# Kernel optimization log

Hardware: AMD Instinct MI355X
Metric: run time of the kernel (lower is better)

## Reference

```python
import jax, jax.numpy as jnp
import numpy as np


def setup_inputs() -> dict:
    key = jax.random.key(0)
    k1, k2, k3 = jax.random.split(key, 3)
    shape = (32, 3, 512, 512)
    inp = jax.random.normal(k1, shape, dtype=jnp.float32)
    tgt = jax.random.normal(k2, shape, dtype=jnp.float32)
    mask = jax.random.randint(k3, shape, 0, 2, dtype=jnp.int32)
    return {"input": inp, "target": tgt, "mask": mask}


def reference(input, target, mask):
    # masked MSE: mean of squared diff over elements where mask == 1
    diff2 = (input - target) ** 2
    m = (mask == 1).astype(diff2.dtype)
    sum2 = jnp.sum(diff2 * m)
    num = jnp.sum(m)
    return sum2 / num
```

## Files before the change

kernel.cpp:

```cpp
#include <hip/hip_runtime.h>


#define BLOCK 256
#define UNROLL 8
#define MAX_PARTS 8192

typedef float vfloat4 __attribute__((ext_vector_type(4)));
typedef int   vint4   __attribute__((ext_vector_type(4)));

__global__ __launch_bounds__(BLOCK, 2) void masked_mse_stage1(
    const vfloat4* __restrict__ inp,
    const vfloat4* __restrict__ tgt,
    const vint4* __restrict__ msk,
    float* __restrict__ part_sum,
    unsigned int* __restrict__ part_cnt)
{
    const long base = (long)blockIdx.x * (BLOCK * UNROLL) + threadIdx.x;

    vfloat4 a[UNROLL];
    vfloat4 b[UNROLL];
    vint4 m[UNROLL];
#pragma unroll
    for (int u = 0; u < UNROLL; ++u) {
        const long i = base + (long)u * BLOCK;
        a[u] = __builtin_nontemporal_load(&inp[i]);
        b[u] = __builtin_nontemporal_load(&tgt[i]);
        m[u] = __builtin_nontemporal_load(&msk[i]);
    }

    float s = 0.0f;
    unsigned int c = 0u;
#pragma unroll
    for (int u = 0; u < UNROLL; ++u) {
        float d0 = a[u].x - b[u].x;
        float d1 = a[u].y - b[u].y;
        float d2 = a[u].z - b[u].z;
        float d3 = a[u].w - b[u].w;
        s += (float)m[u].x * d0 * d0;
        s += (float)m[u].y * d1 * d1;
        s += (float)m[u].z * d2 * d2;
        s += (float)m[u].w * d3 * d3;
        c += (unsigned int)(m[u].x + m[u].y + m[u].z + m[u].w);
    }

#pragma unroll
    for (int off = 32; off > 0; off >>= 1) {
        s += __shfl_down(s, off, 64);
        c += __shfl_down(c, off, 64);
    }

    __shared__ float ssum[BLOCK / 64];
    __shared__ unsigned int scnt[BLOCK / 64];
    const int lane = threadIdx.x & 63;
    const int wave = threadIdx.x >> 6;
    if (lane == 0) {
        ssum[wave] = s;
        scnt[wave] = c;
    }
    __syncthreads();
    if (threadIdx.x == 0) {
        float bs = 0.0f;
        unsigned int bc = 0u;
#pragma unroll
        for (int w = 0; w < BLOCK / 64; ++w) {
            bs += ssum[w];
            bc += scnt[w];
        }
        part_sum[blockIdx.x] = bs;
        part_cnt[blockIdx.x] = bc;
    }
}

__global__ void masked_mse_tail(
    const float* __restrict__ inp,
    const float* __restrict__ tgt,
    const int* __restrict__ msk,
    float* __restrict__ part_sum,
    unsigned int* __restrict__ part_cnt,
    long start, long n, int tail_base)
{
    long i = start + blockIdx.x * (long)blockDim.x + threadIdx.x;
    float s = 0.0f;
    unsigned int c = 0u;
    for (; i < n; i += (long)gridDim.x * blockDim.x) {
        float d = inp[i] - tgt[i];
        int mv = msk[i];
        s += (float)mv * d * d;
        c += (unsigned int)mv;
    }
#pragma unroll
    for (int off = 32; off > 0; off >>= 1) {
        s += __shfl_down(s, off, 64);
        c += __shfl_down(c, off, 64);
    }
    __shared__ float ssum[4];
    __shared__ unsigned int scnt[4];
    const int lane = threadIdx.x & 63;
    const int wave = threadIdx.x >> 6;
    if (lane == 0) { ssum[wave] = s; scnt[wave] = c; }
    __syncthreads();
    if (threadIdx.x == 0) {
        float bs = 0.0f;
        unsigned int bc = 0u;
        for (int w = 0; w < (int)(blockDim.x / 64); ++w) { bs += ssum[w]; bc += scnt[w]; }
        part_sum[tail_base + blockIdx.x] = bs;
        part_cnt[tail_base + blockIdx.x] = bc;
    }
}

__global__ __launch_bounds__(1024) void masked_mse_stage2(
    const float* __restrict__ part_sum,
    const unsigned int* __restrict__ part_cnt,
    int nparts,
    float* __restrict__ out)
{
    float s = 0.0f;
    unsigned int c = 0u;
    for (int i = threadIdx.x; i < nparts; i += blockDim.x) {
        s += part_sum[i];
        c += part_cnt[i];
    }
#pragma unroll
    for (int off = 32; off > 0; off >>= 1) {
        s += __shfl_down(s, off, 64);
        c += __shfl_down(c, off, 64);
    }
    __shared__ float ssum[16];
    __shared__ unsigned int scnt[16];
    const int lane = threadIdx.x & 63;
    const int wave = threadIdx.x >> 6;
    if (lane == 0) { ssum[wave] = s; scnt[wave] = c; }
    __syncthreads();
    if (threadIdx.x == 0) {
        float ts = 0.0f;
        unsigned int tc = 0u;
#pragma unroll
        for (int w = 0; w < 16; ++w) { ts += ssum[w]; tc += scnt[w]; }
        out[0] = ts / (float)tc;
    }
}

extern "C" void kernel_launch(void* const* d_in, const int* in_sizes, int n_in,
                              void* d_out, int out_size, void* d_ws, size_t ws_size,
                              hipStream_t stream)
{
    const float* inp = (const float*)d_in[0];
    const float* tgt = (const float*)d_in[1];
    const int* msk = (const int*)d_in[2];
    const long n = in_sizes[0];
    const long n4 = n / 4;

    float* part_sum = (float*)d_ws;
    unsigned int* part_cnt = (unsigned int*)((char*)d_ws + MAX_PARTS * sizeof(float));

    const long per_block = (long)BLOCK * UNROLL;
    long nblocks = n4 / per_block;
    if (nblocks > MAX_PARTS - 64) nblocks = MAX_PARTS - 64;

    int nparts = 0;
    if (nblocks > 0) {
        masked_mse_stage1<<<(int)nblocks, BLOCK, 0, stream>>>(
            (const vfloat4*)inp, (const vfloat4*)tgt, (const vint4*)msk,
            part_sum, part_cnt);
        nparts = (int)nblocks;
    }
    const long covered = nblocks * per_block * 4;
    if (covered < n) {
        masked_mse_tail<<<64, BLOCK, 0, stream>>>(
            inp, tgt, msk, part_sum, part_cnt, covered, n, nparts);
        nparts += 64;
    }
    masked_mse_stage2<<<1, 1024, 0, stream>>>(part_sum, part_cnt, nparts, (float*)d_out);
}
```

Baseline: 246.6 us.

## Fuse final reduction into main kernel via hierarchical atomic tickets

Replaces the separate stage-2 reduction launch with a last-block-done pattern. Each block writes its partial sum and count as a packed float2 with an agent-scope atomic store, then takes a ticket from one of eight group counters and a second-level counter. The last block reads all partials and writes the mean. This removes a kernel launch and its gap, at the cost of a memset launch, per-block atomics and a serial final reduction in one block. Counts are now accumulated in float.

```diff
diff --git a/kernel.cpp b/kernel.cpp
--- a/kernel.cpp
+++ b/kernel.cpp
@@ -6,15 +6,39 @@
 #define MAX_PARTS 8192
 
 typedef float vfloat4 __attribute__((ext_vector_type(4)));
+typedef float vfloat2 __attribute__((ext_vector_type(2)));
 typedef int   vint4   __attribute__((ext_vector_type(4)));
 
-__global__ __launch_bounds__(BLOCK, 2) void masked_mse_stage1(
+__device__ __forceinline__ void store_part_agent(vfloat2* p, float s, float c)
+{
+    vfloat2 v; v.x = s; v.y = c;
+    unsigned long long u = __builtin_bit_cast(unsigned long long, v);
+    __hip_atomic_store((unsigned long long*)p, u, __ATOMIC_RELAXED,
+                       __HIP_MEMORY_SCOPE_AGENT);
+}
+__device__ __forceinline__ vfloat2 load_part_agent(const vfloat2* p)
+{
+    unsigned long long u = __hip_atomic_load((const unsigned long long*)p,
+                                             __ATOMIC_RELAXED,
+                                             __HIP_MEMORY_SCOPE_AGENT);
+    return __builtin_bit_cast(vfloat2, u);
+}
+
+template <int FINISH>
+__global__ __launch_bounds__(BLOCK, 2) void masked_mse_fused(
     const vfloat4* __restrict__ inp,
     const vfloat4* __restrict__ tgt,
     const vint4* __restrict__ msk,
-    float* __restrict__ part_sum,
-    unsigned int* __restrict__ part_cnt)
-{
+    vfloat2* __restrict__ parts,
+    unsigned int* __restrict__ tickets,
+    float* __restrict__ out)
+{
+    __shared__ float ssum[BLOCK / 64];
+    __shared__ unsigned int scnt[BLOCK / 64];
+    __shared__ int amLast;
+    __shared__ float f1[BLOCK / 64];
+    __shared__ float f2[BLOCK / 64];
+
     const long base = (long)blockIdx.x * (BLOCK * UNROLL) + threadIdx.x;
 
     vfloat4 a[UNROLL];
@@ -49,8 +73,6 @@
         c += __shfl_down(c, off, 64);
     }
 
-    __shared__ float ssum[BLOCK / 64];
-    __shared__ unsigned int scnt[BLOCK / 64];
     const int lane = threadIdx.x & 63;
     const int wave = threadIdx.x >> 6;
     if (lane == 0) {
@@ -58,6 +80,7 @@
         scnt[wave] = c;
     }
     __syncthreads();
+
     if (threadIdx.x == 0) {
         float bs = 0.0f;
         unsigned int bc = 0u;
@@ -66,8 +89,51 @@
             bs += ssum[w];
             bc += scnt[w];
         }
-        part_sum[blockIdx.x] = bs;
-        part_cnt[blockIdx.x] = bc;
+        store_part_agent(&parts[blockIdx.x], bs, (float)bc);
+
+        if (FINISH) {
+            const unsigned int g = blockIdx.x & 7u;
+            const unsigned int nb = gridDim.x;
+            const unsigned int gsz = nb / 8u + (g < (nb & 7u) ? 1u : 0u);
+            int last = 0;
+            unsigned int old = __hip_atomic_fetch_add(
+                &tickets[g], 1u, __ATOMIC_ACQ_REL, __HIP_MEMORY_SCOPE_AGENT);
+            if (old == gsz - 1u) {
+                const unsigned int ng = nb < 8u ? nb : 8u;
+                unsigned int o2 = __hip_atomic_fetch_add(
+                    &tickets[8], 1u, __ATOMIC_ACQ_REL, __HIP_MEMORY_SCOPE_AGENT);
+                last = (o2 == ng - 1u) ? 1 : 0;
+            }
+            amLast = last;
+        } else {
+            amLast = 0;
+        }
+    }
+
+    if (FINISH) {
+        __syncthreads();
+        if (amLast) {
+            float fs = 0.0f;
+            float fc = 0.0f;
+            for (unsigned int i = threadIdx.x; i < gridDim.x; i += BLOCK) {
+                vfloat2 p = load_part_agent(&parts[i]);
+                fs += p.x;
+                fc += p.y;
+            }
+#pragma unroll
+            for (int off = 32; off > 0; off >>= 1) {
+                fs += __shfl_down(fs, off, 64);
+                fc += __shfl_down(fc, off, 64);
+            }
+            if (lane == 0) { f1[wave] = fs; f2[wave] = fc; }
+            __syncthreads();
+            if (threadIdx.x == 0) {
+                float ts = 0.0f, tc = 0.0f;
+#pragma unroll
+                for (int w = 0; w < BLOCK / 64; ++w) { ts += f1[w]; tc += f2[w]; }
+                out[0] = ts / tc;
+            }
+        }
     }
 }
 
@@ -75,8 +141,7 @@
     const float* __restrict__ inp,
     const float* __restrict__ tgt,
     const int* __restrict__ msk,
-    float* __restrict__ part_sum,
-    unsigned int* __restrict__ part_cnt,
+    vfloat2* __restrict__ parts,
     long start, long n, int tail_base)
 {
     long i = start + blockIdx.x * (long)blockDim.x + threadIdx.x;
@@ -103,40 +168,39 @@
         float bs = 0.0f;
         unsigned int bc = 0u;
         for (int w = 0; w < (int)(blockDim.x / 64); ++w) { bs += ssum[w]; bc += scnt[w]; }
-        part_sum[tail_base + blockIdx.x] = bs;
-        part_cnt[tail_base + blockIdx.x] = bc;
-    }
-}
-
-__global__ __launch_bounds__(1024) void masked_mse_stage2(
-    const float* __restrict__ part_sum,
-    const unsigned int* __restrict__ part_cnt,
+        vfloat2 p; p.x = bs; p.y = (float)bc;
+        parts[tail_base + blockIdx.x] = p;
+    }
+}
+
+__global__ __launch_bounds__(256) void masked_mse_stage2(
+    const vfloat2* __restrict__ parts,
     int nparts,
     float* __restrict__ out)
 {
     float s = 0.0f;
-    unsigned int c = 0u;
+    float c = 0.0f;
     for (int i = threadIdx.x; i < nparts; i += blockDim.x) {
-        s += part_sum[i];
-        c += part_cnt[i];
+        vfloat2 p = parts[i];
+        s += p.x;
+        c += p.y;
     }
 #pragma unroll
     for (int off = 32; off > 0; off >>= 1) {
         s += __shfl_down(s, off, 64);
         c += __shfl_down(c, off, 64);
     }
-    __shared__ float ssum[16];
-    __shared__ unsigned int scnt[16];
+    __shared__ float ssum[4];
+    __shared__ float scnt[4];
     const int lane = threadIdx.x & 63;
     const int wave = threadIdx.x >> 6;
     if (lane == 0) { ssum[wave] = s; scnt[wave] = c; }
     __syncthreads();
     if (threadIdx.x == 0) {
-        float ts = 0.0f;
-        unsigned int tc = 0u;
-#pragma unroll
-        for (int w = 0; w < 16; ++w) { ts += ssum[w]; tc += scnt[w]; }
-        out[0] = ts / (float)tc;
+        float ts = 0.0f, tc = 0.0f;
+#pragma unroll
+        for (int w = 0; w < 4; ++w) { ts += ssum[w]; tc += scnt[w]; }
+        out[0] = ts / tc;
     }
 }
 
@@ -150,25 +214,34 @@
     const long n = in_sizes[0];
     const long n4 = n / 4;
 
-    float* part_sum = (float*)d_ws;
-    unsigned int* part_cnt = (unsigned int*)((char*)d_ws + MAX_PARTS * sizeof(float));
+    vfloat2* parts = (vfloat2*)d_ws;
+    unsigned int* tickets =
+        (unsigned int*)((char*)d_ws + (size_t)MAX_PARTS * sizeof(vfloat2));
 
     const long per_block = (long)BLOCK * UNROLL;
     long nblocks = n4 / per_block;
     if (nblocks > MAX_PARTS - 64) nblocks = MAX_PARTS - 64;
+    const long covered = nblocks * per_block * 4;
+
+    if (nblocks > 0 && covered == n) {
+        hipMemsetAsync(tickets, 0, 64, stream);
+        masked_mse_fused<1><<<(int)nblocks, BLOCK, 0, stream>>>(
+            (const vfloat4*)inp, (const vfloat4*)tgt, (const vint4*)msk,
+            parts, tickets, (float*)d_out);
+        return;
+    }
 
     int nparts = 0;
     if (nblocks > 0) {
-        masked_mse_stage1<<<(int)nblocks, BLOCK, 0, stream>>>(
+        masked_mse_fused<0><<<(int)nblocks, BLOCK, 0, stream>>>(
             (const vfloat4*)inp, (const vfloat4*)tgt, (const vint4*)msk,
-            part_sum, part_cnt);
+            parts, tickets, (float*)d_out);
         nparts = (int)nblocks;
     }
-    const long covered = nblocks * per_block * 4;
     if (covered < n) {
         masked_mse_tail<<<64, BLOCK, 0, stream>>>(
-            inp, tgt, msk, part_sum, part_cnt, covered, n, nparts);
+            inp, tgt, msk, parts, covered, n, nparts);
         nparts += 64;
     }
-    masked_mse_stage2<<<1, 1024, 0, stream>>>(part_sum, part_cnt, nparts, (float*)d_out);
-}
+    masked_mse_stage2<<<1, 256, 0, stream>>>(parts, nparts, (float*)d_out);
+}
```

After: 403.3 us. +63.5%, slower.
